# Kernel optimization log

Measured on AMD Instinct MI355X. Metric: run time of the kernel, lower is better.

Reference implementation:

```python
import jax, jax.numpy as jnp
import numpy as np

E, U, D, R = 200000, 50000, 128, 32
N2, N1, NU = 100000, 80000, 20000  # hop-2 frontier, hop-1 frontier, unreachable; N1+N2+NU == E
M1, M0 = 1600000, 800000


def setup_inputs() -> dict:
    key = jax.random.key(0)
    ks = jax.random.split(key, 16)
    inp = {
        'ent_emb': jax.random.normal(ks[0], (E, D), jnp.float32) * 0.1,
        'user_emb': jax.random.normal(ks[1], (U, D), jnp.float32) * 0.1,
        'rel_emb': jax.random.normal(ks[2], (R, D), jnp.float32) * 0.1,
        'W_self': jax.random.normal(ks[3], (D, D), jnp.float32) / np.sqrt(D),
        'W_nei': jax.random.normal(ks[4], (D, D), jnp.float32) / np.sqrt(D),
        'b': jnp.zeros((D,), jnp.float32),
        'final_indices': jax.random.randint(ks[5], (N2,), 0, E, jnp.int32),
        'ent_now1': jax.random.randint(ks[6], (N1,), 0, E, jnp.int32),
        'e1_src': jax.random.randint(ks[7], (M1,), 0, N2, jnp.int32),
        'e1_dst': jax.random.randint(ks[8], (M1,), 0, N1, jnp.int32),
        'e1_rel': jax.random.randint(ks[9], (M1,), 0, R, jnp.int32),
        'e0_src': jax.random.randint(ks[10], (M0,), 0, N1, jnp.int32),
        'e0_dst': jax.random.randint(ks[11], (M0,), 0, U, jnp.int32),
        'e0_rel': jax.random.randint(ks[12], (M0,), 0, R, jnp.int32),
        'unreach_idx': jax.random.randint(ks[13], (NU,), 0, E, jnp.int32),
        'order': jax.random.permutation(ks[14], E).astype(jnp.int32),
    }
    return inp


def _rgcn_layer(x, tail, src, dst, rel, W_self, W_nei, b, rel_emb, n_out, activate):
    # self transform: [N, D]
    out = x @ W_self + b
    if tail is not None:
        # gather neighbor reps + relation modulation: [M, D]
        msg = tail[src] * rel_emb[rel]
        agg = jax.ops.segment_sum(msg, dst, num_segments=n_out)
        deg = jax.ops.segment_sum(jnp.ones_like(dst, dtype=x.dtype), dst, num_segments=n_out)
        agg = agg / jnp.clip(deg, 1.0)[:, None]
        out = out + agg @ W_nei
    return jnp.tanh(out) if activate else out


def reference(ent_emb, user_emb, rel_emb, W_self, W_nei, b,
              final_indices, ent_now1, e1_src, e1_dst, e1_rel,
              e0_src, e0_dst, e0_rel, unreach_idx, order):
    # hop 2: raw gathered entity embeddings (deepest frontier)
    h2 = ent_emb[final_indices]                                            # [N2, D]
    # hop 1: RGCN over kg edges from hop-2 frontier
    h1 = _rgcn_layer(ent_emb[ent_now1], h2, e1_src, e1_dst, e1_rel,
                     W_self, W_nei, b, rel_emb, N1, activate=True)          # [N1, D]
    # hop 0: user representations, no activation (activate=False in source)
    user_rep = _rgcn_layer(user_emb, h1, e0_src, e0_dst, e0_rel,
                           W_self, W_nei, b, rel_emb, U, activate=False)    # [U, D]
    # unreachable entities: self-only transform (tail_rep=None)
    unreachable = _rgcn_layer(ent_emb[unreach_idx], None, None, None, None,
                              W_self, W_nei, b, rel_emb, NU, activate=True)  # [NU, D]
    # concat hop reps in forward hop order, then reindex-scatter by entity order
    ent_user_all = jnp.concatenate([h1, h2, unreachable], axis=0)[order]    # [E, D]
    return jnp.concatenate([user_rep, ent_user_all], axis=0)               # [U+E, D]
```

## Files before the change

kernel.cpp:

```cpp
#include <hip/hip_runtime.h>

#define E_  200000
#define U_  50000
#define D_  128
#define R_  32
#define N2_ 100000
#define N1_ 80000
#define NU_ 20000
#define M1_ 1600000
#define M0_ 800000

#define NBUCK1 313
#define NBUCK0 196

__device__ __forceinline__ float4 ld4(const float* p) {
    return *reinterpret_cast<const float4*>(p);
}
__device__ __forceinline__ void st4(float* p, float4 v) {
    *reinterpret_cast<float4*>(p) = v;
}

__device__ __forceinline__ float fast_tanh(float x) {
    float e = __expf(2.0f * x);
    return 1.0f - 2.0f / (e + 1.0f);
}

__global__ __launch_bounds__(256) void gather_rows_k(
    const float* __restrict__ src, const int* __restrict__ idx,
    float* __restrict__ out, int n)
{
    long long gid = (long long)blockIdx.x * blockDim.x + threadIdx.x;
    int i = (int)(gid >> 5);
    int l = (int)(gid & 31);
    if (i >= n) return;
    int s = idx[i];
    st4(out + (long long)i * 128 + l * 4, ld4(src + (long long)s * 128 + l * 4));
}

__global__ __launch_bounds__(256) void hist_k(
    const int* __restrict__ dst, int* __restrict__ cnt, int M)
{
    int i = blockIdx.x * blockDim.x + threadIdx.x;
    if (i < M) atomicAdd(&cnt[dst[i]], 1);
}

__global__ __launch_bounds__(256) void partial_sums_k(
    const int* __restrict__ cnt, int* __restrict__ bsum, int N)
{
    __shared__ int sm[256];
    const int t = threadIdx.x;
    const int base = blockIdx.x * 1024;
    int sum = 0;
    #pragma unroll
    for (int i = 0; i < 4; ++i) {
        int g = base + t + i * 256;
        if (g < N) sum += cnt[g];
    }
    sm[t] = sum;
    __syncthreads();
    #pragma unroll
    for (int s = 128; s > 0; s >>= 1) {
        if (t < s) sm[t] += sm[t + s];
        __syncthreads();
    }
    if (t == 0) bsum[blockIdx.x] = sm[0];
}

__global__ __launch_bounds__(256) void scan_partials_k(
    int* __restrict__ bsum, int NB, int* __restrict__ off, int N)
{
    __shared__ int ls[256];
    const int t = threadIdx.x;
    int v = (t < NB) ? bsum[t] : 0;
    ls[t] = v;
    __syncthreads();
    #pragma unroll
    for (int d = 1; d < 256; d <<= 1) {
        int u = (t >= d) ? ls[t - d] : 0;
        __syncthreads();
        ls[t] += u;
        __syncthreads();
    }
    if (t < NB) bsum[t] = ls[t] - v;
    if (t == 255) off[N] = ls[255];
}

__global__ __launch_bounds__(256) void scan_apply_k(
    const int* __restrict__ cnt, const int* __restrict__ bsum,
    int* __restrict__ off, int* __restrict__ cur, int N)
{
    __shared__ int buf[1024];
    __shared__ int ts[256];
    const int t = threadIdx.x;
    const int base = blockIdx.x * 1024;
    #pragma unroll
    for (int i = 0; i < 4; ++i) {
        int g = base + t + i * 256;
        buf[t + i * 256] = (g < N) ? cnt[g] : 0;
    }
    __syncthreads();
    const int a = buf[t * 4], b = buf[t * 4 + 1], c = buf[t * 4 + 2], d = buf[t * 4 + 3];
    const int s = a + b + c + d;
    ts[t] = s;
    __syncthreads();
    #pragma unroll
    for (int dd = 1; dd < 256; dd <<= 1) {
        int u = (t >= dd) ? ts[t - dd] : 0;
        __syncthreads();
        ts[t] += u;
        __syncthreads();
    }
    const int pre = bsum[blockIdx.x] + ts[t] - s;
    const int o0 = pre, o1 = pre + a, o2 = o1 + b, o3 = o2 + c;
    const int g0 = base + t * 4;
    if (g0 + 3 < N) {
        *reinterpret_cast<int4*>(off + g0) = make_int4(o0, o1, o2, o3);
        *reinterpret_cast<int4*>(cur + g0) = make_int4(o0, o1, o2, o3);
    } else {
        if (g0     < N) { off[g0]     = o0; cur[g0]     = o0; }
        if (g0 + 1 < N) { off[g0 + 1] = o1; cur[g0 + 1] = o1; }
        if (g0 + 2 < N) { off[g0 + 2] = o2; cur[g0 + 2] = o2; }
    }
}

__global__ __launch_bounds__(256) void init_bcur_k(
    const int* __restrict__ off, int* __restrict__ bcur, int nbuck)
{
    int i = blockIdx.x * blockDim.x + threadIdx.x;
    if (i < nbuck) bcur[i] = off[i << 8];
}

#define EPB 2048
__global__ __launch_bounds__(256) void bin_k(
    const int* __restrict__ src, const int* __restrict__ dst,
    const int* __restrict__ rel, int* __restrict__ bcur,
    int* __restrict__ bdst, int* __restrict__ bsr, int M, int nbuck)
{
    __shared__ int hist[384];
    __shared__ int base[384];
    const int t = threadIdx.x;
    const int e0 = blockIdx.x * EPB;
    for (int i = t; i < nbuck; i += 256) hist[i] = 0;
    __syncthreads();
    int dv[8], sv[8], rv[8];
    #pragma unroll
    for (int i = 0; i < 8; ++i) {
        int e = e0 + i * 256 + t;
        if (e < M) {
            dv[i] = dst[e]; sv[i] = src[e]; rv[i] = rel[e];
            atomicAdd(&hist[dv[i] >> 8], 1);
        } else dv[i] = -1;
    }
    __syncthreads();
    for (int i = t; i < nbuck; i += 256) {
        int c = hist[i];
        base[i] = c ? atomicAdd(&bcur[i], c) : 0;
        hist[i] = 0;
    }
    __syncthreads();
    #pragma unroll
    for (int i = 0; i < 8; ++i) {
        if (dv[i] >= 0) {
            int bk = dv[i] >> 8;
            int p = base[bk] + atomicAdd(&hist[bk], 1);
            bdst[p] = dv[i];
            bsr[p] = sv[i] | (rv[i] << 20);
        }
    }
}

__global__ __launch_bounds__(256) void fill2_k(
    const int* __restrict__ bdst, const int* __restrict__ bsr,
    const int* __restrict__ off, int* __restrict__ cur,
    int* __restrict__ sorted, int N)
{
    int b = blockIdx.x;
    int rs = off[b << 8];
    int reidx = (b + 1) << 8;
    if (reidx > N) reidx = N;
    int re = off[reidx];
    for (int j = rs + threadIdx.x; j < re; j += 256) {
        int d = bdst[j];
        int p = atomicAdd(&cur[d], 1);
        sorted[p] = bsr[j];
    }
}

__global__ __launch_bounds__(256) void seg_reduce_k(
    const float* __restrict__ tail, const float* __restrict__ rel_emb,
    const int* __restrict__ off, const int* __restrict__ sorted,
    float* __restrict__ aggout, int N)
{
    long long gid = (long long)blockIdx.x * blockDim.x + threadIdx.x;
    int row = (int)(gid >> 5);
    int l = (int)(gid & 31) * 4;
    if (row >= N) return;
    int s = off[row], e = off[row + 1];
    float4 acc = make_float4(0.f, 0.f, 0.f, 0.f);
    int j = s;
    for (; j + 1 < e; j += 2) {
        int p0 = sorted[j], p1 = sorted[j + 1];
        float4 t0 = ld4(tail + (long long)(p0 & 0xFFFFF) * 128 + l);
        float4 r0 = ld4(rel_emb + (long long)(p0 >> 20) * 128 + l);
        float4 t1 = ld4(tail + (long long)(p1 & 0xFFFFF) * 128 + l);
        float4 r1 = ld4(rel_emb + (long long)(p1 >> 20) * 128 + l);
        acc.x = fmaf(t0.x, r0.x, acc.x); acc.y = fmaf(t0.y, r0.y, acc.y);
        acc.z = fmaf(t0.z, r0.z, acc.z); acc.w = fmaf(t0.w, r0.w, acc.w);
        acc.x = fmaf(t1.x, r1.x, acc.x); acc.y = fmaf(t1.y, r1.y, acc.y);
        acc.z = fmaf(t1.z, r1.z, acc.z); acc.w = fmaf(t1.w, r1.w, acc.w);
    }
    if (j < e) {
        int p0 = sorted[j];
        float4 t0 = ld4(tail + (long long)(p0 & 0xFFFFF) * 128 + l);
        float4 r0 = ld4(rel_emb + (long long)(p0 >> 20) * 128 + l);
        acc.x = fmaf(t0.x, r0.x, acc.x); acc.y = fmaf(t0.y, r0.y, acc.y);
        acc.z = fmaf(t0.z, r0.z, acc.z); acc.w = fmaf(t0.w, r0.w, acc.w);
    }
    float sc = 1.0f / (float)max(e - s, 1);
    acc.x *= sc; acc.y *= sc; acc.z *= sc; acc.w *= sc;
    st4(aggout + (long long)row * 128 + l, acc);
}

template<bool GATHER, bool ACCUM, bool BIAS, bool ACT>
__global__ __launch_bounds__(256) void gemm_rows_k(
    const float* __restrict__ X, const int* __restrict__ idx,
    const float* __restrict__ W, const float* __restrict__ bias,
    float* __restrict__ Out, int N)
{
    __shared__ float XsT[32][128];
    __shared__ float Ws [32][128];
    const int tid = threadIdx.x;
    const int rowbase = blockIdx.x * 128;
    const int r0 = (tid >> 4) * 8;
    const int c0 = (tid & 15) * 8;

    float acc[8][8];
    if (BIAS) {
        #pragma unroll
        for (int j = 0; j < 8; ++j) {
            float bv = bias[c0 + j];
            #pragma unroll
            for (int i = 0; i < 8; ++i) acc[i][j] = bv;
        }
    } else {
        #pragma unroll
        for (int i = 0; i < 8; ++i)
            #pragma unroll
            for (int j = 0; j < 8; ++j) acc[i][j] = 0.0f;
    }

    const int srow = tid >> 3;
    const int skq  = (tid & 7) * 4;
    const int sswz = (tid & 7) << 2;
    const int wkk  = tid >> 5;
    const int wcc  = (tid & 31) * 4;

    for (int k0 = 0; k0 < 128; k0 += 32) {
        __syncthreads();
        #pragma unroll
        for (int p = 0; p < 4; ++p) {
            int row = p * 32 + srow;
            int grow = rowbase + row;
            int cl = grow < N ? grow : (N - 1);
            const float* xr = GATHER ? X + (long long)idx[cl] * 128
                                     : X + (long long)cl * 128;
            float4 v = ld4(xr + k0 + skq);
            int rs = row ^ sswz;
            XsT[skq + 0][rs] = v.x;
            XsT[skq + 1][rs] = v.y;
            XsT[skq + 2][rs] = v.z;
            XsT[skq + 3][rs] = v.w;
        }
        #pragma unroll
        for (int p = 0; p < 4; ++p) {
            int k = p * 8 + wkk;
            st4(&Ws[k][wcc], ld4(W + (long long)(k0 + k) * 128 + wcc));
        }
        __syncthreads();
        #pragma unroll
        for (int k = 0; k < 32; ++k) {
            int A0 = (((r0 >> 2) ^ ((k >> 2) & 7)) << 2);
            float4 x0 = ld4(&XsT[k][A0]);
            float4 x1 = ld4(&XsT[k][A0 ^ 4]);
            float4 w0 = ld4(&Ws[k][c0]);
            float4 w1 = ld4(&Ws[k][c0 + 4]);
            float xs[8] = {x0.x, x0.y, x0.z, x0.w, x1.x, x1.y, x1.z, x1.w};
            float ws[8] = {w0.x, w0.y, w0.z, w0.w, w1.x, w1.y, w1.z, w1.w};
            #pragma unroll
            for (int i = 0; i < 8; ++i)
                #pragma unroll
                for (int j = 0; j < 8; ++j)
                    acc[i][j] = fmaf(xs[i], ws[j], acc[i][j]);
        }
    }

    #pragma unroll
    for (int i = 0; i < 8; ++i) {
        int row = rowbase + r0 + i;
        if (row >= N) continue;
        float* op = Out + (long long)row * 128 + c0;
        float vals[8];
        #pragma unroll
        for (int j = 0; j < 8; ++j) vals[j] = acc[i][j];
        if (ACCUM) {
            float4 o0 = ld4(op), o1 = ld4(op + 4);
            vals[0] += o0.x; vals[1] += o0.y; vals[2] += o0.z; vals[3] += o0.w;
            vals[4] += o1.x; vals[5] += o1.y; vals[6] += o1.z; vals[7] += o1.w;
        }
        if (ACT) {
            #pragma unroll
            for (int j = 0; j < 8; ++j) vals[j] = fast_tanh(vals[j]);
        }
        st4(op,     make_float4(vals[0], vals[1], vals[2], vals[3]));
        st4(op + 4, make_float4(vals[4], vals[5], vals[6], vals[7]));
    }
}

template<bool GATHER1, bool ACT>
__global__ __launch_bounds__(256) void gemm_fused_k(
    const float* __restrict__ X1, const int* __restrict__ idx,
    const float* __restrict__ X2,
    const float* __restrict__ W1, const float* __restrict__ W2,
    const float* __restrict__ bias, float* __restrict__ Out, int N)
{
    __shared__ float X1sT[32][128];
    __shared__ float X2sT[32][128];
    __shared__ float W1s [32][128];
    __shared__ float W2s [32][128];
    const int tid = threadIdx.x;
    const int rowbase = blockIdx.x * 128;
    const int r0 = (tid >> 4) * 8;
    const int c0 = (tid & 15) * 8;

    float acc[8][8];
    #pragma unroll
    for (int j = 0; j < 8; ++j) {
        float bv = bias[c0 + j];
        #pragma unroll
        for (int i = 0; i < 8; ++i) acc[i][j] = bv;
    }

    const int srow = tid >> 3;
    const int skq  = (tid & 7) * 4;
    const int sswz = (tid & 7) << 2;
    const int wkk  = tid >> 5;
    const int wcc  = (tid & 31) * 4;

    for (int k0 = 0; k0 < 128; k0 += 32) {
        __syncthreads();
        #pragma unroll
        for (int p = 0; p < 4; ++p) {
            int row = p * 32 + srow;
            int grow = rowbase + row;
            int cl = grow < N ? grow : (N - 1);
            const float* x1r = GATHER1 ? X1 + (long long)idx[cl] * 128
                                       : X1 + (long long)cl * 128;
            const float* x2r = X2 + (long long)cl * 128;
            float4 v1 = ld4(x1r + k0 + skq);
            float4 v2 = ld4(x2r + k0 + skq);
            int rs = row ^ sswz;
            X1sT[skq + 0][rs] = v1.x; X1sT[skq + 1][rs] = v1.y;
            X1sT[skq + 2][rs] = v1.z; X1sT[skq + 3][rs] = v1.w;
            X2sT[skq + 0][rs] = v2.x; X2sT[skq + 1][rs] = v2.y;
            X2sT[skq + 2][rs] = v2.z; X2sT[skq + 3][rs] = v2.w;
        }
        #pragma unroll
        for (int p = 0; p < 4; ++p) {
            int k = p * 8 + wkk;
            st4(&W1s[k][wcc], ld4(W1 + (long long)(k0 + k) * 128 + wcc));
            st4(&W2s[k][wcc], ld4(W2 + (long long)(k0 + k) * 128 + wcc));
        }
        __syncthreads();
        #pragma unroll
        for (int k = 0; k < 32; ++k) {
            int A0 = (((r0 >> 2) ^ ((k >> 2) & 7)) << 2);
            float4 a0 = ld4(&X1sT[k][A0]);
            float4 a1 = ld4(&X1sT[k][A0 ^ 4]);
            float4 b0 = ld4(&X2sT[k][A0]);
            float4 b1 = ld4(&X2sT[k][A0 ^ 4]);
            float4 u0 = ld4(&W1s[k][c0]);
            float4 u1 = ld4(&W1s[k][c0 + 4]);
            float4 v0 = ld4(&W2s[k][c0]);
            float4 v1 = ld4(&W2s[k][c0 + 4]);
            float x1s[8] = {a0.x, a0.y, a0.z, a0.w, a1.x, a1.y, a1.z, a1.w};
            float x2s[8] = {b0.x, b0.y, b0.z, b0.w, b1.x, b1.y, b1.z, b1.w};
            float w1s[8] = {u0.x, u0.y, u0.z, u0.w, u1.x, u1.y, u1.z, u1.w};
            float w2s[8] = {v0.x, v0.y, v0.z, v0.w, v1.x, v1.y, v1.z, v1.w};
            #pragma unroll
            for (int i = 0; i < 8; ++i)
                #pragma unroll
                for (int j = 0; j < 8; ++j) {
                    acc[i][j] = fmaf(x1s[i], w1s[j], acc[i][j]);
                    acc[i][j] = fmaf(x2s[i], w2s[j], acc[i][j]);
                }
        }
    }

    #pragma unroll
    for (int i = 0; i < 8; ++i) {
        int row = rowbase + r0 + i;
        if (row >= N) continue;
        float* op = Out + (long long)row * 128 + c0;
        float vals[8];
        #pragma unroll
        for (int j = 0; j < 8; ++j) vals[j] = acc[i][j];
        if (ACT) {
            #pragma unroll
            for (int j = 0; j < 8; ++j) vals[j] = fast_tanh(vals[j]);
        }
        st4(op,     make_float4(vals[0], vals[1], vals[2], vals[3]));
        st4(op + 4, make_float4(vals[4], vals[5], vals[6], vals[7]));
    }
}

extern "C" void kernel_launch(void* const* d_in, const int* in_sizes, int n_in,
                              void* d_out, int out_size, void* d_ws, size_t ws_size,
                              hipStream_t stream)
{
    const float* ent_emb  = (const float*)d_in[0];
    const float* user_emb = (const float*)d_in[1];
    const float* rel_emb  = (const float*)d_in[2];
    const float* W_self   = (const float*)d_in[3];
    const float* W_nei    = (const float*)d_in[4];
    const float* bvec     = (const float*)d_in[5];
    const int* final_indices = (const int*)d_in[6];
    const int* ent_now1   = (const int*)d_in[7];
    const int* e1_src     = (const int*)d_in[8];
    const int* e1_dst     = (const int*)d_in[9];
    const int* e1_rel     = (const int*)d_in[10];
    const int* e0_src     = (const int*)d_in[11];
    const int* e0_dst     = (const int*)d_in[12];
    const int* e0_rel     = (const int*)d_in[13];
    const int* unreach_idx = (const int*)d_in[14];
    const int* order      = (const int*)d_in[15];

    float* out = (float*)d_out;
    float* ws  = (float*)d_ws;

    float* concat = ws;
    float* agg1 = concat + (size_t)E_ * 128;
    float* agg0 = agg1 + (size_t)N1_ * 128;
    int* cur1 = (int*)(agg0 + (size_t)U_ * 128);
    int* cur0 = cur1 + N1_;
    int* off1 = cur0 + U_;
    int* off0 = off1 + (N1_ + 4);
    int* bsum1 = off0 + (U_ + 4);
    int* bsum0 = bsum1 + 256;
    int* bcur1 = bsum0 + 256;
    int* bcur0 = bcur1 + 320;
    int* sorted1 = bcur0 + 320;
    int* sorted0 = sorted1 + M1_;

    int* bdst = (int*)agg1;
    int* bsr  = bdst + M1_;

    float* h1   = concat;
    float* h2   = concat + (size_t)N1_ * 128;
    float* unre = concat + (size_t)(N1_ + N2_) * 128;

    const int NB1 = (N1_ + 1023) / 1024;
    const int NB0 = (U_  + 1023) / 1024;

    hipMemsetAsync(cur1, 0, (size_t)(N1_ + U_) * sizeof(int), stream);

    gather_rows_k<<<(N2_ * 32 + 255) / 256, 256, 0, stream>>>(
        ent_emb, final_indices, h2, N2_);

    hist_k<<<(M1_ + 255) / 256, 256, 0, stream>>>(e1_dst, cur1, M1_);
    partial_sums_k<<<NB1, 256, 0, stream>>>(cur1, bsum1, N1_);
    scan_partials_k<<<1, 256, 0, stream>>>(bsum1, NB1, off1, N1_);
    scan_apply_k<<<NB1, 256, 0, stream>>>(cur1, bsum1, off1, cur1, N1_);
    init_bcur_k<<<2, 256, 0, stream>>>(off1, bcur1, NBUCK1);
    bin_k<<<(M1_ + EPB - 1) / EPB, 256, 0, stream>>>(
        e1_src, e1_dst, e1_rel, bcur1, bdst, bsr, M1_, NBUCK1);
    fill2_k<<<NBUCK1, 256, 0, stream>>>(bdst, bsr, off1, cur1, sorted1, N1_);
    seg_reduce_k<<<(N1_ * 32 + 255) / 256, 256, 0, stream>>>(
        h2, rel_emb, off1, sorted1, agg1, N1_);

    gemm_fused_k<true, true><<<(N1_ + 127) / 128, 256, 0, stream>>>(
        ent_emb, ent_now1, agg1, W_self, W_nei, bvec, h1, N1_);

    hist_k<<<(M0_ + 255) / 256, 256, 0, stream>>>(e0_dst, cur0, M0_);
    partial_sums_k<<<NB0, 256, 0, stream>>>(cur0, bsum0, U_);
    scan_partials_k<<<1, 256, 0, stream>>>(bsum0, NB0, off0, U_);
    scan_apply_k<<<NB0, 256, 0, stream>>>(cur0, bsum0, off0, cur0, U_);
    init_bcur_k<<<1, 256, 0, stream>>>(off0, bcur0, NBUCK0);
    bin_k<<<(M0_ + EPB - 1) / EPB, 256, 0, stream>>>(
        e0_src, e0_dst, e0_rel, bcur0, bdst, bsr, M0_, NBUCK0);
    fill2_k<<<NBUCK0, 256, 0, stream>>>(bdst, bsr, off0, cur0, sorted0, U_);
    seg_reduce_k<<<(U_ * 32 + 255) / 256, 256, 0, stream>>>(
        h1, rel_emb, off0, sorted0, agg0, U_);

    gemm_fused_k<false, false><<<(U_ + 127) / 128, 256, 0, stream>>>(
        user_emb, nullptr, agg0, W_self, W_nei, bvec, out, U_);

    gemm_rows_k<true, false, true, true><<<(NU_ + 127) / 128, 256, 0, stream>>>(
        ent_emb, unreach_idx, W_self, bvec, unre, NU_);

    gather_rows_k<<<(E_ * 32 + 255) / 256, 256, 0, stream>>>(
        concat, order, out + (size_t)U_ * 128, E_);
}
```

Measured before the change: 931.9 us.

## Restructure fused GEMM as concatenated-K loop with halved LDS and split columns

The two-operand fused GEMM is rewritten to treat [X1|X2]·[W1;W2] as one K=256 GEMM, staging one 32-wide chunk at a time. This halves shared memory and register pressure per block, allowing more resident blocks per CU (launch bounds now request 4). Each thread's columns are split into c4 and c4+64 to spread LDS bank access, and gather indices are hoisted out of the K loop. In exchange the kernel runs twice as many K iterations, each with its own barriers.

Measured after the change: 988.7 us. +6.1%, slower.

```diff
diff --git a/kernel.cpp b/kernel.cpp
--- a/kernel.cpp
+++ b/kernel.cpp
@@ -221,8 +221,8 @@
     st4(aggout + (long long)row * 128 + l, acc);
 }
 
-template<bool GATHER, bool ACCUM, bool BIAS, bool ACT>
-__global__ __launch_bounds__(256) void gemm_rows_k(
+template<bool GATHER, bool BIAS, bool ACT>
+__global__ __launch_bounds__(256, 4) void gemm_rows_k(
     const float* __restrict__ X, const int* __restrict__ idx,
     const float* __restrict__ W, const float* __restrict__ bias,
     float* __restrict__ Out, int N)
@@ -232,21 +232,14 @@
     const int tid = threadIdx.x;
     const int rowbase = blockIdx.x * 128;
     const int r0 = (tid >> 4) * 8;
-    const int c0 = (tid & 15) * 8;
+    const int c4 = (tid & 15) * 4;
 
     float acc[8][8];
-    if (BIAS) {
-        #pragma unroll
-        for (int j = 0; j < 8; ++j) {
-            float bv = bias[c0 + j];
-            #pragma unroll
-            for (int i = 0; i < 8; ++i) acc[i][j] = bv;
-        }
-    } else {
-        #pragma unroll
-        for (int i = 0; i < 8; ++i)
-            #pragma unroll
-            for (int j = 0; j < 8; ++j) acc[i][j] = 0.0f;
+    #pragma unroll
+    for (int j = 0; j < 8; ++j) {
+        float bv = BIAS ? bias[(j < 4) ? (c4 + j) : (c4 + 64 + j - 4)] : 0.0f;
+        #pragma unroll
+        for (int i = 0; i < 8; ++i) acc[i][j] = bv;
     }
 
     const int srow = tid >> 3;
@@ -255,17 +248,20 @@
     const int wkk  = tid >> 5;
     const int wcc  = (tid & 31) * 4;
 
+    int cl[4], gi[4];
+    #pragma unroll
+    for (int p = 0; p < 4; ++p) {
+        int grow = rowbase + p * 32 + srow;
+        cl[p] = grow < N ? grow : (N - 1);
+        gi[p] = GATHER ? idx[cl[p]] : cl[p];
+    }
+
     for (int k0 = 0; k0 < 128; k0 += 32) {
         __syncthreads();
         #pragma unroll
         for (int p = 0; p < 4; ++p) {
-            int row = p * 32 + srow;
-            int grow = rowbase + row;
-            int cl = grow < N ? grow : (N - 1);
-            const float* xr = GATHER ? X + (long long)idx[cl] * 128
-                                     : X + (long long)cl * 128;
-            float4 v = ld4(xr + k0 + skq);
-            int rs = row ^ sswz;
+            float4 v = ld4(X + (long long)gi[p] * 128 + k0 + skq);
+            int rs = (p * 32 + srow) ^ sswz;
             XsT[skq + 0][rs] = v.x;
             XsT[skq + 1][rs] = v.y;
             XsT[skq + 2][rs] = v.z;
@@ -282,8 +278,8 @@
             int A0 = (((r0 >> 2) ^ ((k >> 2) & 7)) << 2);
             float4 x0 = ld4(&XsT[k][A0]);
             float4 x1 = ld4(&XsT[k][A0 ^ 4]);
-            float4 w0 = ld4(&Ws[k][c0]);
-            float4 w1 = ld4(&Ws[k][c0 + 4]);
+            float4 w0 = ld4(&Ws[k][c4]);
+            float4 w1 = ld4(&Ws[k][c4 + 64]);
             float xs[8] = {x0.x, x0.y, x0.z, x0.w, x1.x, x1.y, x1.z, x1.w};
             float ws[8] = {w0.x, w0.y, w0.z, w0.w, w1.x, w1.y, w1.z, w1.w};
             #pragma unroll
@@ -298,44 +294,37 @@
     for (int i = 0; i < 8; ++i) {
         int row = rowbase + r0 + i;
         if (row >= N) continue;
-        float* op = Out + (long long)row * 128 + c0;
+        float* op = Out + (long long)row * 128;
         float vals[8];
         #pragma unroll
         for (int j = 0; j < 8; ++j) vals[j] = acc[i][j];
-        if (ACCUM) {
-            float4 o0 = ld4(op), o1 = ld4(op + 4);
-            vals[0] += o0.x; vals[1] += o0.y; vals[2] += o0.z; vals[3] += o0.w;
-            vals[4] += o1.x; vals[5] += o1.y; vals[6] += o1.z; vals[7] += o1.w;
-        }
         if (ACT) {
             #pragma unroll
             for (int j = 0; j < 8; ++j) vals[j] = fast_tanh(vals[j]);
         }
-        st4(op,     make_float4(vals[0], vals[1], vals[2], vals[3]));
-        st4(op + 4, make_float4(vals[4], vals[5], vals[6], vals[7]));
+        st4(op + c4,      make_float4(vals[0], vals[1], vals[2], vals[3]));
+        st4(op + c4 + 64, make_float4(vals[4], vals[5], vals[6], vals[7]));
     }
 }
 
 template<bool GATHER1, bool ACT>
-__global__ __launch_bounds__(256) void gemm_fused_k(
+__global__ __launch_bounds__(256, 4) void gemm_cat_k(
     const float* __restrict__ X1, const int* __restrict__ idx,
     const float* __restrict__ X2,
     const float* __restrict__ W1, const float* __restrict__ W2,
     const float* __restrict__ bias, float* __restrict__ Out, int N)
 {
-    __shared__ float X1sT[32][128];
-    __shared__ float X2sT[32][128];
-    __shared__ float W1s [32][128];
-    __shared__ float W2s [32][128];
+    __shared__ float XsT[32][128];
+    __shared__ float Ws [32][128];
     const int tid = threadIdx.x;
     const int rowbase = blockIdx.x * 128;
     const int r0 = (tid >> 4) * 8;
-    const int c0 = (tid & 15) * 8;
+    const int c4 = (tid & 15) * 4;
 
     float acc[8][8];
     #pragma unroll
     for (int j = 0; j < 8; ++j) {
-        float bv = bias[c0 + j];
+        float bv = bias[(j < 4) ? (c4 + j) : (c4 + 64 + j - 4)];
         #pragma unroll
         for (int i = 0; i < 8; ++i) acc[i][j] = bv;
     }
@@ -346,53 +335,51 @@
     const int wkk  = tid >> 5;
     const int wcc  = (tid & 31) * 4;
 
-    for (int k0 = 0; k0 < 128; k0 += 32) {
+    int cl[4], gi[4];
+    #pragma unroll
+    for (int p = 0; p < 4; ++p) {
+        int grow = rowbase + p * 32 + srow;
+        cl[p] = grow < N ? grow : (N - 1);
+        gi[p] = GATHER1 ? idx[cl[p]] : cl[p];
+    }
+
+    for (int cc = 0; cc < 8; ++cc) {
         __syncthreads();
         #pragma unroll
         for (int p = 0; p < 4; ++p) {
-            int row = p * 32 + srow;
-            int grow = rowbase + row;
-            int cl = grow < N ? grow : (N - 1);
-            const float* x1r = GATHER1 ? X1 + (long long)idx[cl] * 128
-                                       : X1 + (long long)cl * 128;
-            const float* x2r = X2 + (long long)cl * 128;
-            float4 v1 = ld4(x1r + k0 + skq);
-            float4 v2 = ld4(x2r + k0 + skq);
-            int rs = row ^ sswz;
-            X1sT[skq + 0][rs] = v1.x; X1sT[skq + 1][rs] = v1.y;
-            X1sT[skq + 2][rs] = v1.z; X1sT[skq + 3][rs] = v1.w;
-            X2sT[skq + 0][rs] = v2.x; X2sT[skq + 1][rs] = v2.y;
-            X2sT[skq + 2][rs] = v2.z; X2sT[skq + 3][rs] = v2.w;
+            const float* xr;
+            if (cc < 4) xr = X1 + (long long)gi[p] * 128 + cc * 32;
+            else        xr = X2 + (long long)cl[p] * 128 + (cc - 4) * 32;
+            float4 v = ld4(xr + skq);
+            int rs = (p * 32 + srow) ^ sswz;
+            XsT[skq + 0][rs] = v.x;
+            XsT[skq + 1][rs] = v.y;
+            XsT[skq + 2][rs] = v.z;
+            XsT[skq + 3][rs] = v.w;
         }
         #pragma unroll
         for (int p = 0; p < 4; ++p) {
             int k = p * 8 + wkk;
-            st4(&W1s[k][wcc], ld4(W1 + (long long)(k0 + k) * 128 + wcc));
-            st4(&W2s[k][wcc], ld4(W2 + (long long)(k0 + k) * 128 + wcc));
+            const float* wsrc = (cc < 4)
+                ? (W1 + (long long)(cc * 32 + k) * 128)
+                : (W2 + (long long)((cc - 4) * 32 + k) * 128);
+            st4(&Ws[k][wcc], ld4(wsrc + wcc));
         }
         __syncthreads();
         #pragma unroll
         for (int k = 0; k < 32; ++k) {
             int A0 = (((r0 >> 2) ^ ((k >> 2) & 7)) << 2);
-            float4 a0 = ld4(&X1sT[k][A0]);
-            float4 a1 = ld4(&X1sT[k][A0 ^ 4]);
-            float4 b0 = ld4(&X2sT[k][A0]);
-            float4 b1 = ld4(&X2sT[k][A0 ^ 4]);
-            float4 u0 = ld4(&W1s[k][c0]);
-            float4 u1 = ld4(&W1s[k][c0 + 4]);
-            float4 v0 = ld4(&W2s[k][c0]);
-            float4 v1 = ld4(&W2s[k][c0 + 4]);
-            float x1s[8] = {a0.x, a0.y, a0.z, a0.w, a1.x, a1.y, a1.z, a1.w};
-            float x2s[8] = {b0.x, b0.y, b0.z, b0.w, b1.x, b1.y, b1.z, b1.w};
-            float w1s[8] = {u0.x, u0.y, u0.z, u0.w, u1.x, u1.y, u1.z, u1.w};
-            float w2s[8] = {v0.x, v0.y, v0.z, v0.w, v1.x, v1.y, v1.z, v1.w};
+            float4 x0 = ld4(&XsT[k][A0]);
+            float4 x1 = ld4(&XsT[k][A0 ^ 4]);
+            float4 w0 = ld4(&Ws[k][c4]);
+            float4 w1 = ld4(&Ws[k][c4 + 64]);
+            float xs[8] = {x0.x, x0.y, x0.z, x0.w, x1.x, x1.y, x1.z, x1.w};
+            float ws[8] = {w0.x, w0.y, w0.z, w0.w, w1.x, w1.y, w1.z, w1.w};
             #pragma unroll
             for (int i = 0; i < 8; ++i)
                 #pragma unroll
-                for (int j = 0; j < 8; ++j) {
-                    acc[i][j] = fmaf(x1s[i], w1s[j], acc[i][j]);
-                    acc[i][j] = fmaf(x2s[i], w2s[j], acc[i][j]);
-                }
+                for (int j = 0; j < 8; ++j)
+                    acc[i][j] = fmaf(xs[i], ws[j], acc[i][j]);
         }
     }
 
@@ -400,7 +387,7 @@
     for (int i = 0; i < 8; ++i) {
         int row = rowbase + r0 + i;
         if (row >= N) continue;
-        float* op = Out + (long long)row * 128 + c0;
+        float* op = Out + (long long)row * 128;
         float vals[8];
         #pragma unroll
         for (int j = 0; j < 8; ++j) vals[j] = acc[i][j];
@@ -408,8 +395,8 @@
             #pragma unroll
             for (int j = 0; j < 8; ++j) vals[j] = fast_tanh(vals[j]);
         }
-        st4(op,     make_float4(vals[0], vals[1], vals[2], vals[3]));
-        st4(op + 4, make_float4(vals[4], vals[5], vals[6], vals[7]));
+        st4(op + c4,      make_float4(vals[0], vals[1], vals[2], vals[3]));
+        st4(op + c4 + 64, make_float4(vals[4], vals[5], vals[6], vals[7]));
     }
 }
 
@@ -477,7 +464,7 @@
     seg_reduce_k<<<(N1_ * 32 + 255) / 256, 256, 0, stream>>>(
         h2, rel_emb, off1, sorted1, agg1, N1_);
 
-    gemm_fused_k<true, true><<<(N1_ + 127) / 128, 256, 0, stream>>>(
+    gemm_cat_k<true, true><<<(N1_ + 127) / 128, 256, 0, stream>>>(
         ent_emb, ent_now1, agg1, W_self, W_nei, bvec, h1, N1_);
 
     hist_k<<<(M0_ + 255) / 256, 256, 0, stream>>>(e0_dst, cur0, M0_);
@@ -491,10 +478,10 @@
     seg_reduce_k<<<(U_ * 32 + 255) / 256, 256, 0, stream>>>(
         h1, rel_emb, off0, sorted0, agg0, U_);
 
-    gemm_fused_k<false, false><<<(U_ + 127) / 128, 256, 0, stream>>>(
+    gemm_cat_k<false, false><<<(U_ + 127) / 128, 256, 0, stream>>>(
         user_emb, nullptr, agg0, W_self, W_nei, bvec, out, U_);
 
-    gemm_rows_k<true, false, true, true><<<(NU_ + 127) / 128, 256, 0, stream>>>(
+    gemm_rows_k<true, true, true><<<(NU_ + 127) / 128, 256, 0, stream>>>(
         ent_emb, unreach_idx, W_self, bvec, unre, NU_);
 
     gather_rows_k<<<(E_ * 32 + 255) / 256, 256, 0, stream>>>(
```
